# Optimization experiments

Measured on AMD Instinct MI355X. Metric: run time of the kernel, lower is better.

Reference implementation:

```python
import jax, jax.numpy as jnp
import numpy as np

N_NODES = 100000
FEAT = 256
EMBED = 128
K = 10          # sampled neighbors per node (num_sample)
E = 4096        # edge batch
NUM_CLASSES = 2


def setup_inputs() -> dict:
    key = jax.random.key(0)
    ks = jax.random.split(key, 6)
    edges = jax.random.randint(ks[0], (E, 2), 0, N_NODES)
    neigh_idx = jax.random.randint(ks[1], (N_NODES, K), 0, N_NODES)
    features = jax.random.normal(ks[2], (N_NODES, FEAT), dtype=jnp.float32)
    W1 = jax.random.normal(ks[3], (EMBED, FEAT), dtype=jnp.float32) * (FEAT ** -0.5)
    W2 = jax.random.normal(ks[4], (EMBED, EMBED), dtype=jnp.float32) * (EMBED ** -0.5)
    Wc = jax.random.normal(ks[5], (NUM_CLASSES, EMBED), dtype=jnp.float32) * (EMBED ** -0.5)
    return {"edges": edges, "neigh_idx": neigh_idx, "features": features,
            "W1": W1, "W2": W2, "Wc": Wc}


def reference(edges, neigh_idx, features, W1, W2, Wc):
    # 2-layer GraphSage-style encoder (gcn mean aggregation), batched over E edges.
    idx2 = neigh_idx[edges]              # [E,2,K]   1-hop neighbors of edge endpoints
    idx1 = neigh_idx[idx2]               # [E,2,K,K] 2-hop neighbors
    # layer 1: mean of raw features over 2-hop neighbor sets, then linear + relu
    f1 = jnp.mean(features[idx1], axis=3)                 # [E,2,K,FEAT]
    h1 = jax.nn.relu(jnp.einsum('epkf,df->epkd', f1, W1)) # [E,2,K,EMBED]
    # layer 2: mean over 1-hop neighbors, then linear (last encoder: no relu)
    h1m = jnp.mean(h1, axis=2)                            # [E,2,EMBED]
    h2 = jnp.einsum('epd,gd->epg', h1m, W2)               # [E,2,EMBED]
    # edge pooling ('mean'): average the two endpoint embeddings
    pooled = 0.5 * (h2[:, 0] + h2[:, 1])                  # [E,EMBED]
    # classifier: weight.mm(embeds).t()
    return pooled @ Wc.T                                  # [E,NUM_CLASSES]
```

## Files before the change

kernel.cpp:

```cpp
#include <hip/hip_runtime.h>
#include <hip/hip_bf16.h>


typedef __bf16 bf16x8 __attribute__((ext_vector_type(8)));
typedef float f32x4 __attribute__((ext_vector_type(4)));

#define FEAT 256
#define EMB  128
#define KNB  10
#define BM   128

__device__ inline unsigned short f2b(float f) {
  unsigned int u = __float_as_uint(f);
  unsigned int r = (u + 0x7fffu + ((u >> 16) & 1u)) >> 16;
  return (unsigned short)r;
}
__device__ inline float b2f(unsigned short s) {
  return __uint_as_float(((unsigned int)s) << 16);
}


__global__ void setup(const float* __restrict__ W1, const float* __restrict__ W2,
                      const float* __restrict__ Wc,
                      unsigned short* __restrict__ w1b, float* __restrict__ M2) {
  const int b = blockIdx.x;
  if (b < 128) {
    int i = b * 256 + threadIdx.x;
    w1b[i] = f2b(W1[i]);
  } else {
    int t = threadIdx.x, c = t >> 7, d = t & 127;
    float s = 0.f;
    for (int g = 0; g < EMB; ++g) s += Wc[c * EMB + g] * W2[g * EMB + d];
    M2[t] = s;
  }
}


__global__ __launch_bounds__(512, 4) void gemm_z(
    const float* __restrict__ feat, const unsigned short* __restrict__ w1b,
    unsigned short* __restrict__ z, int M) {
  __shared__ unsigned short As[BM][FEAT + 8];

  const int wid  = threadIdx.x >> 6;
  const int lane = threadIdx.x & 63;
  const int m0   = blockIdx.x * BM;

  bf16x8 bfrag[8];
  {
    const int col = wid * 16 + (lane & 15);
    const int kof = (lane >> 4) * 8;
#pragma unroll
    for (int kk = 0; kk < 8; ++kk)
      bfrag[kk] = *reinterpret_cast<const bf16x8*>(&w1b[col * FEAT + kk * 32 + kof]);
  }

  const float4* f4 = reinterpret_cast<const float4*>(feat);
  for (int i = threadIdx.x; i < BM * 64; i += 512) {
    int r = i >> 6, c4 = i & 63;
    int row = m0 + r;
    float4 v = make_float4(0.f, 0.f, 0.f, 0.f);
    if (row < M) v = f4[(size_t)row * 64 + c4];
    ushort4 bq;
    bq.x = f2b(v.x); bq.y = f2b(v.y); bq.z = f2b(v.z); bq.w = f2b(v.w);
    *reinterpret_cast<ushort4*>(&As[r][c4 * 4]) = bq;
  }
  __syncthreads();

  f32x4 acc[BM / 16] = {};
  const int arow = lane & 15;
  const int kof  = (lane >> 4) * 8;
#pragma unroll
  for (int mt = 0; mt < BM / 16; ++mt) {
#pragma unroll
    for (int kk = 0; kk < 8; ++kk) {
      bf16x8 a = *reinterpret_cast<const bf16x8*>(&As[mt * 16 + arow][kk * 32 + kof]);
      acc[mt] = __builtin_amdgcn_mfma_f32_16x16x32_bf16(a, bfrag[kk], acc[mt], 0, 0, 0);
    }
  }

  const int col = wid * 16 + (lane & 15);
#pragma unroll
  for (int mt = 0; mt < BM / 16; ++mt) {
    int rbase = m0 + mt * 16 + (lane >> 4) * 4;
#pragma unroll
    for (int r = 0; r < 4; ++r) {
      int row = rbase + r;
      if (row < M) z[(size_t)row * EMB + col] = f2b(acc[mt][r]);
    }
  }
}


__global__ __launch_bounds__(128) void aggregate(
    const int* __restrict__ edges, const int* __restrict__ nidx,
    const unsigned short* __restrict__ z, const float* __restrict__ M2,
    float* __restrict__ out, int E) {
  __shared__ int   s_idx2[2][KNB];
  __shared__ int   s_idx1[2][KNB * KNB];
  __shared__ float s_pm[2][EMB];

  const int e = blockIdx.x;
  const int t = threadIdx.x;
  const int w = t >> 6;
  const int l = t & 63;

  if (t < 2 * KNB) {
    int p = t / KNB, k = t % KNB;
    int v = edges[e * 2 + p];
    s_idx2[p][k] = nidx[(size_t)v * KNB + k];
  }
  __syncthreads();
  for (int i = t; i < 2 * KNB * KNB; i += 128) {
    int p = i / 100, r = i % 100;
    s_idx1[p][r] = nidx[(size_t)s_idx2[p][r / KNB] * KNB + (r % KNB)];
  }
  __syncthreads();

  float pooled0 = 0.f, pooled1 = 0.f;
#pragma unroll
  for (int k = 0; k < KNB; ++k) {
    float a0 = 0.f, a1 = 0.f;
#pragma unroll
    for (int j = 0; j < KNB; ++j) {
      int u = s_idx1[w][k * KNB + j];
      unsigned int q = *reinterpret_cast<const unsigned int*>(&z[(size_t)u * EMB + 2 * l]);
      a0 += b2f((unsigned short)(q & 0xffffu));
      a1 += b2f((unsigned short)(q >> 16));
    }
    pooled0 += fmaxf(a0 * 0.1f, 0.f);
    pooled1 += fmaxf(a1 * 0.1f, 0.f);
  }
  s_pm[w][2 * l]     = pooled0 * 0.1f;
  s_pm[w][2 * l + 1] = pooled1 * 0.1f;
  __syncthreads();

  if (w == 0) {
    int d0 = 2 * l, d1 = 2 * l + 1;
    float p0 = 0.5f * (s_pm[0][d0] + s_pm[1][d0]);
    float p1 = 0.5f * (s_pm[0][d1] + s_pm[1][d1]);
    float s0 = p0 * M2[d0]       + p1 * M2[d1];
    float s1 = p0 * M2[EMB + d0] + p1 * M2[EMB + d1];
#pragma unroll
    for (int off = 32; off > 0; off >>= 1) {
      s0 += __shfl_down(s0, off);
      s1 += __shfl_down(s1, off);
    }
    if (l == 0) { out[e * 2 + 0] = s0; out[e * 2 + 1] = s1; }
  }
}


extern "C" void kernel_launch(void* const* d_in, const int* in_sizes, int n_in,
                              void* d_out, int out_size, void* d_ws, size_t ws_size,
                              hipStream_t stream) {
  const int*   edges = (const int*)d_in[0];
  const int*   nidx  = (const int*)d_in[1];
  const float* feat  = (const float*)d_in[2];
  const float* W1    = (const float*)d_in[3];
  const float* W2    = (const float*)d_in[4];
  const float* Wc    = (const float*)d_in[5];
  float* out = (float*)d_out;

  const int N = in_sizes[2] / FEAT;
  const int E = in_sizes[0] / 2;

  char* ws = (char*)d_ws;
  unsigned short* z   = (unsigned short*)ws;
  size_t zbytes = (size_t)N * EMB * sizeof(unsigned short);
  unsigned short* w1b = (unsigned short*)(ws + zbytes);
  float* M2 = (float*)(ws + zbytes + (size_t)EMB * FEAT * sizeof(unsigned short));

  setup  <<<129, 256, 0, stream>>>(W1, W2, Wc, w1b, M2);
  gemm_z <<<(N + BM - 1) / BM, 512, 0, stream>>>(feat, w1b, z, N);
  aggregate<<<E, 128, 0, stream>>>(edges, nidx, z, M2, out, E);
}
```

Baseline: 214.7 us.

## Fold setup kernel into GEMM and widen aggregate loads to 8 bytes

```diff
diff --git a/kernel.cpp b/kernel.cpp
--- a/kernel.cpp
+++ b/kernel.cpp
@@ -15,31 +15,27 @@
   unsigned int r = (u + 0x7fffu + ((u >> 16) & 1u)) >> 16;
   return (unsigned short)r;
 }
-__device__ inline float b2f(unsigned short s) {
-  return __uint_as_float(((unsigned int)s) << 16);
-}
-
-
-__global__ void setup(const float* __restrict__ W1, const float* __restrict__ W2,
-                      const float* __restrict__ Wc,
-                      unsigned short* __restrict__ w1b, float* __restrict__ M2) {
-  const int b = blockIdx.x;
-  if (b < 128) {
-    int i = b * 256 + threadIdx.x;
-    w1b[i] = f2b(W1[i]);
-  } else {
-    int t = threadIdx.x, c = t >> 7, d = t & 127;
-    float s = 0.f;
-    for (int g = 0; g < EMB; ++g) s += Wc[c * EMB + g] * W2[g * EMB + d];
-    M2[t] = s;
-  }
+__device__ inline float b2f(unsigned int s) {
+  return __uint_as_float(s << 16);
 }
 
 
 __global__ __launch_bounds__(512, 4) void gemm_z(
-    const float* __restrict__ feat, const unsigned short* __restrict__ w1b,
-    unsigned short* __restrict__ z, int M) {
+    const float* __restrict__ feat, const float* __restrict__ W1,
+    const float* __restrict__ W2, const float* __restrict__ Wc,
+    unsigned short* __restrict__ z, float* __restrict__ M2, int M) {
   __shared__ unsigned short As[BM][FEAT + 8];
+
+  if (blockIdx.x == gridDim.x - 1) {
+    int t = threadIdx.x;
+    if (t < 256) {
+      int c = t >> 7, d = t & 127;
+      float s = 0.f;
+      for (int g = 0; g < EMB; ++g) s += Wc[c * EMB + g] * W2[g * EMB + d];
+      M2[t] = s;
+    }
+    return;
+  }
 
   const int wid  = threadIdx.x >> 6;
   const int lane = threadIdx.x & 63;
@@ -50,8 +46,15 @@
     const int col = wid * 16 + (lane & 15);
     const int kof = (lane >> 4) * 8;
 #pragma unroll
-    for (int kk = 0; kk < 8; ++kk)
-      bfrag[kk] = *reinterpret_cast<const bf16x8*>(&w1b[col * FEAT + kk * 32 + kof]);
+    for (int kk = 0; kk < 8; ++kk) {
+      const float* src = &W1[col * FEAT + kk * 32 + kof];
+      float4 lo = *reinterpret_cast<const float4*>(src);
+      float4 hi = *reinterpret_cast<const float4*>(src + 4);
+      union { unsigned short s[8]; bf16x8 v; } cvt;
+      cvt.s[0] = f2b(lo.x); cvt.s[1] = f2b(lo.y); cvt.s[2] = f2b(lo.z); cvt.s[3] = f2b(lo.w);
+      cvt.s[4] = f2b(hi.x); cvt.s[5] = f2b(hi.y); cvt.s[6] = f2b(hi.z); cvt.s[7] = f2b(hi.w);
+      bfrag[kk] = cvt.v;
+    }
   }
 
   const float4* f4 = reinterpret_cast<const float4*>(feat);
@@ -103,6 +106,8 @@
   const int t = threadIdx.x;
   const int w = t >> 6;
   const int l = t & 63;
+  const int h = l >> 5;
+  const int q = l & 31;
 
   if (t < 2 * KNB) {
     int p = t / KNB, k = t % KNB;
@@ -116,22 +121,27 @@
   }
   __syncthreads();
 
-  float pooled0 = 0.f, pooled1 = 0.f;
+  float pooled[4] = {0.f, 0.f, 0.f, 0.f};
 #pragma unroll
   for (int k = 0; k < KNB; ++k) {
-    float a0 = 0.f, a1 = 0.f;
+    float a[4] = {0.f, 0.f, 0.f, 0.f};
 #pragma unroll
-    for (int j = 0; j < KNB; ++j) {
-      int u = s_idx1[w][k * KNB + j];
-      unsigned int q = *reinterpret_cast<const unsigned int*>(&z[(size_t)u * EMB + 2 * l]);
-      a0 += b2f((unsigned short)(q & 0xffffu));
-      a1 += b2f((unsigned short)(q >> 16));
+    for (int jp = 0; jp < KNB / 2; ++jp) {
+      int u = s_idx1[w][k * KNB + jp * 2 + h];
+      uint2 v = *reinterpret_cast<const uint2*>(&z[(size_t)u * EMB + q * 4]);
+      a[0] += b2f(v.x & 0xffffu); a[1] += b2f(v.x >> 16);
+      a[2] += b2f(v.y & 0xffffu); a[3] += b2f(v.y >> 16);
     }
-    pooled0 += fmaxf(a0 * 0.1f, 0.f);
-    pooled1 += fmaxf(a1 * 0.1f, 0.f);
+#pragma unroll
+    for (int c = 0; c < 4; ++c) {
+      float s = a[c] + __shfl_xor(a[c], 32);
+      pooled[c] += fmaxf(s * 0.1f, 0.f);
+    }
   }
-  s_pm[w][2 * l]     = pooled0 * 0.1f;
-  s_pm[w][2 * l + 1] = pooled1 * 0.1f;
+  if (h == 0) {
+#pragma unroll
+    for (int c = 0; c < 4; ++c) s_pm[w][q * 4 + c] = pooled[c] * 0.1f;
+  }
   __syncthreads();
 
   if (w == 0) {
@@ -165,12 +175,10 @@
   const int E = in_sizes[0] / 2;
 
   char* ws = (char*)d_ws;
-  unsigned short* z   = (unsigned short*)ws;
-  size_t zbytes = (size_t)N * EMB * sizeof(unsigned short);
-  unsigned short* w1b = (unsigned short*)(ws + zbytes);
-  float* M2 = (float*)(ws + zbytes + (size_t)EMB * FEAT * sizeof(unsigned short));
+  unsigned short* z = (unsigned short*)ws;
+  float* M2 = (float*)(ws + (size_t)N * EMB * sizeof(unsigned short));
 
-  setup  <<<129, 256, 0, stream>>>(W1, W2, Wc, w1b, M2);
-  gemm_z <<<(N + BM - 1) / BM, 512, 0, stream>>>(feat, w1b, z, N);
+  int mtiles = (N + BM - 1) / BM;
+  gemm_z <<<mtiles + 1, 512, 0, stream>>>(feat, W1, W2, Wc, z, M2, N);
   aggregate<<<E, 128, 0, stream>>>(edges, nidx, z, M2, out, E);
 }
```

Result: no change. 211.2 us (-1.6%).
